# Kernel optimization log

Measured on AMD Instinct MI355X. Metric: run time of the kernel, lower is better.

## Reference

```python
import jax, jax.numpy as jnp
import numpy as np
from jax import lax

B, L, H, O, T = 256, 2, 256, 256, 512


def setup_inputs() -> dict:
    key = jax.random.key(0)
    ks = jax.random.split(key, 9)
    s = 0.1  # keep gates out of saturation
    return {
        "x": jax.random.normal(ks[0], (B, 1, H), jnp.float32),
        "h0": jax.random.normal(ks[1], (L, B, H), jnp.float32) * s,
        "c0": jax.random.normal(ks[2], (L, B, H), jnp.float32) * s,
        "W_ih": jax.random.normal(ks[3], (L, 4 * H, H), jnp.float32) * s,
        "W_hh": jax.random.normal(ks[4], (L, 4 * H, H), jnp.float32) * s,
        "b_ih": jax.random.normal(ks[5], (L, 4 * H), jnp.float32) * s,
        "b_hh": jax.random.normal(ks[6], (L, 4 * H), jnp.float32) * s,
        "fc_w": jax.random.normal(ks[7], (O, H), jnp.float32) * s,
        "fc_b": jax.random.normal(ks[8], (O,), jnp.float32) * s,
        "max_length": T,
    }


def _lstm_cell(inp, h, c, Wi, Wh, bi, bh):
    # PyTorch gate order: i, f, g, o
    gates = inp @ Wi.T + h @ Wh.T + bi + bh  # [B, 4H]
    i, f, g, o = jnp.split(gates, 4, axis=-1)
    i = jax.nn.sigmoid(i)
    f = jax.nn.sigmoid(f)
    g = jnp.tanh(g)
    o = jax.nn.sigmoid(o)
    c_new = f * c + i * g
    h_new = o * jnp.tanh(c_new)
    return h_new, c_new


def reference(x, h0, c0, W_ih, W_hh, b_ih, b_hh, fc_w, fc_b, max_length):
    n_layers = W_ih.shape[0]
    xin = x[:, 0, :]  # same single-step input re-fed every iteration

    def step(carry, _):
        h, c = carry  # each [L, B, H]
        inp = xin
        hs, cs = [], []
        for l in range(n_layers):
            hl, cl = _lstm_cell(inp, h[l], c[l], W_ih[l], W_hh[l], b_ih[l], b_hh[l])
            hs.append(hl)
            cs.append(cl)
            inp = hl
        return (jnp.stack(hs), jnp.stack(cs)), inp  # last-layer hidden

    _, outs = lax.scan(step, (h0, c0), None, length=max_length)  # [T, B, H]
    seq = jnp.transpose(outs, (1, 0, 2))  # [B, T, H]
    logits = seq @ fc_w.T + fc_b  # [B, T, O]
    return jax.nn.log_softmax(logits, axis=-1), jax.nn.softmax(logits, axis=-1)
```

## Files before the change

kernel.cpp:

```cpp
#include <hip/hip_runtime.h>

#define TSTEPS 512
#define BATCH  256
#define HID    256
#define OUTC   256

typedef _Float16 half8 __attribute__((ext_vector_type(8)));
typedef float    f32x4 __attribute__((ext_vector_type(4)));
union G16 { unsigned long long u2[2]; unsigned u[4]; half8 h; };

#define H0_SLOTS 16
#define H1_SLOTS 4
#define H0RING_QW (H0_SLOTS*16*16*128)
#define H1RING_QW (H1_SLOTS*16*16*128)

__device__ __forceinline__ float sigf(float x){ return 1.0f/(1.0f+__expf(-x)); }
__device__ __forceinline__ float tanh_(float x){
  float a = fminf(fmaxf(x,-8.0f),8.0f);
  float e = __expf(2.0f*a);
  return (e-1.0f)/(e+1.0f);
}
__device__ __forceinline__ void st64(unsigned long long* p, unsigned long long v){
  __hip_atomic_store(p, v, __ATOMIC_RELAXED, __HIP_MEMORY_SCOPE_AGENT);
}
__device__ __forceinline__ unsigned long long ld64(const unsigned long long* p){
  return __hip_atomic_load(p, __ATOMIC_RELAXED, __HIP_MEMORY_SCOPE_AGENT);
}
__device__ __forceinline__ void st32(unsigned* p, unsigned v){
  __hip_atomic_store(p, v, __ATOMIC_RELAXED, __HIP_MEMORY_SCOPE_AGENT);
}
__device__ __forceinline__ unsigned ld32(const unsigned* p){
  return __hip_atomic_load(p, __ATOMIC_RELAXED, __HIP_MEMORY_SCOPE_AGENT);
}
__device__ __forceinline__ unsigned pack2(float a, float b){
  _Float16 x=(_Float16)a, y=(_Float16)b;
  return (unsigned)__builtin_bit_cast(unsigned short,x)
       | ((unsigned)__builtin_bit_cast(unsigned short,y)<<16);
}

__global__ void prep_convert(const float* __restrict__ Wih, const float* __restrict__ Whh,
                             const float* __restrict__ fcw, const float* __restrict__ bih,
                             const float* __restrict__ bhh,
                             _Float16* __restrict__ wh0, _Float16* __restrict__ wi1,
                             _Float16* __restrict__ wh1, _Float16* __restrict__ fcwh,
                             float* __restrict__ bias1)
{
  int i = blockIdx.x*256 + threadIdx.x;
  wh0[i] = (_Float16)Whh[i];
  wi1[i] = (_Float16)Wih[262144 + i];
  wh1[i] = (_Float16)Whh[262144 + i];
  if (i < 65536) fcwh[i] = (_Float16)fcw[i];
  if (i < 1024)  bias1[i] = bih[1024+i] + bhh[1024+i];
}

__global__ void prep_gx0(const float* __restrict__ x, const float* __restrict__ Wih,
                         const float* __restrict__ bih, const float* __restrict__ bhh,
                         float* __restrict__ gx0)
{
  int gid = blockIdx.x*256 + threadIdx.x;
  int b = gid >> 10, n = gid & 1023;
  const float4* xv = (const float4*)(x + (size_t)b*256);
  const float4* wv = (const float4*)(Wih + (size_t)n*256);
  float s = bih[n] + bhh[n];
  #pragma unroll 8
  for (int k=0;k<64;k++){
    float4 a = xv[k], c = wv[k];
    s += a.x*c.x + a.y*c.y + a.z*c.z + a.w*c.w;
  }
  gx0[gid] = s;
}

__global__ void zero_scratch(unsigned long long* __restrict__ base, int total){
  int i = blockIdx.x*256 + threadIdx.x;
  if (i < total) st64(base + i, 0ull);
}

__global__ __launch_bounds__(512,1) void lstm4(
    const float* __restrict__ gx0, const _Float16* __restrict__ Wh0g,
    const _Float16* __restrict__ Wi1g, const _Float16* __restrict__ Wh1g,
    const float* __restrict__ bias1, const float* __restrict__ h_in,
    const float* __restrict__ c_in, unsigned* __restrict__ seq1dw,
    unsigned long long* __restrict__ h0r, unsigned long long* __restrict__ h1r,
    unsigned* __restrict__ flagC)
{
  __shared__ __align__(16) char Lb[156160];
  _Float16* Ws  = (_Float16*)Lb;
  _Float16* sh0 = (_Float16*)(Lb + 131072);

  const int blk = blockIdx.x, tid = threadIdx.x;
  const int wv = tid>>6, l = tid&63, c16 = l&15, kg = l>>4;

  if (blk < 64){
    const int grp = blk>>2, s = blk&3, b0 = grp*16;
    const int gate = wv>>1, jblk = (wv&1)*32;
    float (*gbuf)[16][66] = (float (*)[16][66])(Lb + 139264);

    for (int idx=tid; idx<8192; idx+=512){
      int row = idx>>5, gr = idx&31;
      int g = row>>6, jl = row&63;
      half8 v = *(const half8*)(Wh0g + ((size_t)(g*256 + s*64 + jl))*256 + gr*8);
      *(half8*)&Ws[row*256 + (gr^(row&7))*8] = v;
    }
    { int row = tid>>5, q = tid&31;
      const float* sp = h_in + (size_t)(b0+row)*256 + q*8;
      half8 v;
      #pragma unroll
      for (int qq=0;qq<8;qq++) v[qq] = (_Float16)sp[qq];
      *(half8*)&sh0[row*256 + (q^(row&7))*8] = v; }
    const int eb = tid>>5, jp = tid&31;
    float cA = c_in[(size_t)(b0+eb)*256 + s*64 + 2*jp];
    float cB = c_in[(size_t)(b0+eb)*256 + s*64 + 2*jp + 1];
    float gxr[2][4];
    #pragma unroll
    for (int nt=0;nt<2;nt++)
      #pragma unroll
      for (int r=0;r<4;r++)
        gxr[nt][r] = gx0[(size_t)(b0 + kg*4 + r)*1024 + gate*256 + s*64 + jblk + nt*16 + c16];
    const int r0 = gate*64 + jblk + c16, r1 = r0 + 16;
    __syncthreads();

    for (int t=0; t<TSTEPS; ++t){
      if (((t&7)==0) && t>=16 && tid<64){
        const unsigned need = (unsigned)(t-8);
        bool ok;
        do {
          unsigned v = need;
          if (tid < 8) v = ld32(&flagC[grp*8 + tid]);
          ok = (v >= need);
        } while (!__all(ok));
      }
      f32x4 acc0 = { gxr[0][0], gxr[0][1], gxr[0][2], gxr[0][3] };
      f32x4 acc1 = { gxr[1][0], gxr[1][1], gxr[1][2], gxr[1][3] };
      #pragma unroll
      for (int kt=0;kt<8;kt++){
        half8 af  = *(const half8*)&sh0[c16*256 + ((kt*4+kg)^(c16&7))*8];
        half8 b0f = *(const half8*)&Ws[r0*256 + ((kt*4+kg)^(r0&7))*8];
        half8 b1f = *(const half8*)&Ws[r1*256 + ((kt*4+kg)^(r1&7))*8];
        acc0 = __builtin_amdgcn_mfma_f32_16x16x32_f16(af, b0f, acc0, 0,0,0);
        acc1 = __builtin_amdgcn_mfma_f32_16x16x32_f16(af, b1f, acc1, 0,0,0);
      }
      #pragma unroll
      for (int r=0;r<4;r++){
        gbuf[gate][kg*4+r][jblk + c16]      = acc0[r];
        gbuf[gate][kg*4+r][jblk + 16 + c16] = acc1[r];
      }
      __syncthreads();
      {
        int j0 = 2*jp, j1 = 2*jp+1;
        float i0 = sigf (gbuf[0][eb][j0]), i1 = sigf (gbuf[0][eb][j1]);
        float f0 = sigf (gbuf[1][eb][j0]), f1 = sigf (gbuf[1][eb][j1]);
        float g0 = tanh_(gbuf[2][eb][j0]), g1 = tanh_(gbuf[2][eb][j1]);
        float o0 = sigf (gbuf[3][eb][j0]), o1 = sigf (gbuf[3][eb][j1]);
        cA = f0*cA + i0*g0;
        cB = f1*cB + i1*g1;
        unsigned pk = pack2(o0*tanh_(cA), o1*tanh_(cB));
        int jg = s*64 + j0;
        *(unsigned*)&sh0[eb*256 + ((jg>>3)^(eb&7))*8 + (jg&7)] = pk;
        st64(&h0r[(((size_t)(t&(H0_SLOTS-1))*16+grp)*16 + eb)*128 + s*32 + jp],
             (((unsigned long long)(unsigned)(t+2))<<32) | pk);
      }
      {
        int row = tid>>5, q = tid&31;
        if ((q>>3) != s){
          const unsigned long long* p =
            h0r + (((size_t)(t&(H0_SLOTS-1))*16+grp)*16 + row)*128 + q*4;
          unsigned tg32 = (unsigned)(t+2);
          unsigned long long v0,v1,v2,v3;
          for(;;){
            v0=ld64(p); v1=ld64(p+1); v2=ld64(p+2); v3=ld64(p+3);
            bool ok = (unsigned)(v0>>32)==tg32 && (unsigned)(v1>>32)==tg32 &&
                      (unsigned)(v2>>32)==tg32 && (unsigned)(v3>>32)==tg32;
            if (__all(ok)) break;
          }
          G16 g; g.u[0]=(unsigned)v0; g.u[1]=(unsigned)v1;
                 g.u[2]=(unsigned)v2; g.u[3]=(unsigned)v3;
          *(half8*)&sh0[row*256 + (q^(row&7))*8] = g.h;
        }
      }
      __syncthreads();
    }
  } else {
    const int bb = blk-64, grp = bb>>3, js = bb&7;
    const int b0 = grp*16, jb = js*32;
    const int gate = wv>>1, jhalf = (wv&1)*16;
    _Float16* sh1 = (_Float16*)(Lb + 139264);
    float (*gbuf)[16][34] = (float (*)[16][34])(Lb + 147456);

    for (int idx=tid; idx<8192; idx+=512){
      int row = idx>>6, gr = idx&63;
      int g = row>>5, jl = row&31;
      size_t nrow = (size_t)(g*256 + jb + jl);
      const _Float16* src = (gr < 32) ? (Wi1g + nrow*256 + gr*8)
                                      : (Wh1g + nrow*256 + (size_t)(gr-32)*8);
      *(half8*)&Ws[row*512 + (gr^(row&7))*8] = *(const half8*)src;
    }
    { int row = tid>>5, q = tid&31;
      const float* sp = h_in + 65536 + (size_t)(b0+row)*256 + q*8;
      half8 v;
      #pragma unroll
      for (int qq=0;qq<8;qq++) v[qq] = (_Float16)sp[qq];
      *(half8*)&sh1[row*256 + (q^(row&7))*8] = v; }
    const int eb = tid>>4, jp = tid&15;
    float cA = 0.f, cB = 0.f;
    if (tid < 256){
      cA = c_in[65536 + (size_t)(b0+eb)*256 + jb + 2*jp];
      cB = c_in[65536 + (size_t)(b0+eb)*256 + jb + 2*jp + 1];
    }
    const float bv = bias1[gate*256 + jb + jhalf + c16];
    const int nl = gate*32 + jhalf + c16;
    const int prow = tid>>5, pq = tid&31;
    unsigned long long hv0,hv1,hv2,hv3;
    {
      const unsigned long long* p = h0r + (((size_t)grp)*16 + prow)*128 + pq*4;
      hv0=ld64(p); hv1=ld64(p+1); hv2=ld64(p+2); hv3=ld64(p+3);
    }
    __syncthreads();

    for (int t=0; t<TSTEPS; ++t){
      {
        unsigned tg32 = (unsigned)(t+2);
        const unsigned long long* p =
          h0r + (((size_t)(t&(H0_SLOTS-1))*16+grp)*16 + prow)*128 + pq*4;
        for(;;){
          bool ok = (unsigned)(hv0>>32)==tg32 && (unsigned)(hv1>>32)==tg32 &&
                    (unsigned)(hv2>>32)==tg32 && (unsigned)(hv3>>32)==tg32;
          if (__all(ok)) break;
          hv0=ld64(p); hv1=ld64(p+1); hv2=ld64(p+2); hv3=ld64(p+3);
        }
        G16 g; g.u[0]=(unsigned)hv0; g.u[1]=(unsigned)hv1;
               g.u[2]=(unsigned)hv2; g.u[3]=(unsigned)hv3;
        *(half8*)&sh0[prow*256 + (pq^(prow&7))*8] = g.h;
      }
      __syncthreads();
      if (((t&7)==0) && tid==0) st32(&flagC[grp*8+js], (unsigned)t);
      f32x4 acc = { bv, bv, bv, bv };
      #pragma unroll
      for (int kt=0;kt<8;kt++){
        half8 af = *(const half8*)&sh0[c16*256 + ((kt*4+kg)^(c16&7))*8];
        half8 bf = *(const half8*)&Ws[nl*512 + ((kt*4+kg)^(nl&7))*8];
        acc = __builtin_amdgcn_mfma_f32_16x16x32_f16(af, bf, acc, 0,0,0);
      }
      if (t > 0 && (pq>>2) != js){
        const unsigned long long* p =
          h1r + (((size_t)((t+3)&(H1_SLOTS-1))*16+grp)*16 + prow)*128 + pq*4;
        unsigned tg32 = (unsigned)(t+1);
        unsigned long long v0,v1,v2,v3;
        for(;;){
          v0=ld64(p); v1=ld64(p+1); v2=ld64(p+2); v3=ld64(p+3);
          bool ok = (unsigned)(v0>>32)==tg32 && (unsigned)(v1>>32)==tg32 &&
                    (unsigned)(v2>>32)==tg32 && (unsigned)(v3>>32)==tg32;
          if (__all(ok)) break;
        }
        G16 g; g.u[0]=(unsigned)v0; g.u[1]=(unsigned)v1;
               g.u[2]=(unsigned)v2; g.u[3]=(unsigned)v3;
        *(half8*)&sh1[prow*256 + (pq^(prow&7))*8] = g.h;
      }
      __syncthreads();
      #pragma unroll
      for (int kt=0;kt<8;kt++){
        half8 af = *(const half8*)&sh1[c16*256 + ((kt*4+kg)^(c16&7))*8];
        half8 bf = *(const half8*)&Ws[nl*512 + ((32+kt*4+kg)^(nl&7))*8];
        acc = __builtin_amdgcn_mfma_f32_16x16x32_f16(af, bf, acc, 0,0,0);
      }
      #pragma unroll
      for (int r=0;r<4;r++) gbuf[gate][kg*4+r][jhalf + c16] = acc[r];
      __syncthreads();
      if (tid < 256){
        int j0 = 2*jp, j1 = 2*jp+1;
        float i0 = sigf (gbuf[0][eb][j0]), i1 = sigf (gbuf[0][eb][j1]);
        float f0 = sigf (gbuf[1][eb][j0]), f1 = sigf (gbuf[1][eb][j1]);
        float g0 = tanh_(gbuf[2][eb][j0]), g1 = tanh_(gbuf[2][eb][j1]);
        float o0 = sigf (gbuf[3][eb][j0]), o1 = sigf (gbuf[3][eb][j1]);
        cA = f0*cA + i0*g0;
        cB = f1*cB + i1*g1;
        unsigned pk = pack2(o0*tanh_(cA), o1*tanh_(cB));
        int jg = jb + j0;
        *(unsigned*)&sh1[eb*256 + ((jg>>3)^(eb&7))*8 + (jg&7)] = pk;
        st64(&h1r[(((size_t)(t&(H1_SLOTS-1))*16+grp)*16 + eb)*128 + js*16 + jp],
             (((unsigned long long)(unsigned)(t+2))<<32) | pk);
        seq1dw[((size_t)(b0+eb)*TSTEPS + t)*256 + js*16 + jp] = pk;
      }
      if (t+1 < TSTEPS){
        const unsigned long long* p =
          h0r + (((size_t)((t+1)&(H0_SLOTS-1))*16+grp)*16 + prow)*128 + pq*4;
        hv0=ld64(p); hv1=ld64(p+1); hv2=ld64(p+2); hv3=ld64(p+3);
      }
    }
  }
}

__global__ __launch_bounds__(256) void fc_kernel(
    const _Float16* __restrict__ seq, int pitch,
    const _Float16* __restrict__ fcwh, const float* __restrict__ fcb,
    float* __restrict__ out0, float* __restrict__ out1)
{
  const int tid = threadIdx.x;
  const int w = tid >> 6, l = tid & 63;
  const int col = l & 15, kg = l >> 4;
  const size_t m0 = (size_t)blockIdx.x*64 + (size_t)w*16;
  half8 a[8];
  #pragma unroll
  for (int kt=0;kt<8;kt++)
    a[kt] = *(const half8*)&seq[(m0+col)*(size_t)pitch + kt*32 + kg*8];
  f32x4 acc[16];
  #pragma unroll
  for (int nt=0;nt<16;nt++){
    int n = nt*16 + col;
    float bvl = fcb[n];
    f32x4 c = {bvl,bvl,bvl,bvl};
    const _Float16* wr = fcwh + (size_t)n*256;
    #pragma unroll
    for (int kt=0;kt<8;kt++){
      half8 bf = *(const half8*)&wr[kt*32 + kg*8];
      c = __builtin_amdgcn_mfma_f32_16x16x32_f16(a[kt], bf, c, 0,0,0);
    }
    acc[nt] = c;
  }
  #pragma unroll
  for (int r=0;r<4;r++){
    float mx = -3.0e38f;
    #pragma unroll
    for (int nt=0;nt<16;nt++) mx = fmaxf(mx, acc[nt][r]);
    #pragma unroll
    for (int off=1; off<16; off<<=1) mx = fmaxf(mx, __shfl_xor(mx, off, 64));
    float s = 0.0f;
    #pragma unroll
    for (int nt=0;nt<16;nt++) s += __expf(acc[nt][r]-mx);
    #pragma unroll
    for (int off=1; off<16; off<<=1) s += __shfl_xor(s, off, 64);
    float inv = 1.0f/s;
    float ls  = __logf(s);
    size_t row = m0 + (size_t)kg*4 + r;
    #pragma unroll
    for (int nt=0;nt<16;nt++){
      int n = nt*16 + col;
      float v = acc[nt][r]-mx;
      out0[row*256 + n] = v - ls;
      out1[row*256 + n] = __expf(v)*inv;
    }
  }
}

extern "C" void kernel_launch(void* const* d_in, const int* in_sizes, int n_in,
                              void* d_out, int out_size, void* d_ws, size_t ws_size,
                              hipStream_t stream)
{
  const float* x   = (const float*)d_in[0];
  const float* h0  = (const float*)d_in[1];
  const float* c0  = (const float*)d_in[2];
  const float* Wih = (const float*)d_in[3];
  const float* Whh = (const float*)d_in[4];
  const float* bih = (const float*)d_in[5];
  const float* bhh = (const float*)d_in[6];
  const float* fcw = (const float*)d_in[7];
  const float* fcb = (const float*)d_in[8];
  (void)in_sizes; (void)n_in; (void)out_size; (void)ws_size;

  char* ws = (char*)d_ws;
  _Float16* wh0   = (_Float16*)(ws + 0);
  _Float16* wi1   = (_Float16*)(ws + (512<<10));
  _Float16* wh1   = (_Float16*)(ws + (1024<<10));
  _Float16* fcwh  = (_Float16*)(ws + (1536<<10));
  float*    bias1 = (float*)   (ws + (1664<<10));
  float*    gx0   = (float*)   (ws + (1668<<10));

  char* ob = (char*)d_out;
  float* out0 = (float*)d_out;
  float* out1 = out0 + (size_t)BATCH*TSTEPS*OUTC;
  unsigned long long* h0r   = (unsigned long long*)ob;
  unsigned long long* h1r   = h0r + H0RING_QW;
  unsigned*           flagC = (unsigned*)(h1r + H1RING_QW);
  unsigned* seq1dw = (unsigned*)out1;
  _Float16* seq1   = (_Float16*)out1;

  const int zeroQW = H0RING_QW + H1RING_QW + 64;
  hipLaunchKernelGGL(zero_scratch, dim3((zeroQW+255)/256), dim3(256), 0, stream,
                     h0r, zeroQW);
  hipLaunchKernelGGL(prep_convert, dim3(1024), dim3(256), 0, stream,
                     Wih, Whh, fcw, bih, bhh, wh0, wi1, wh1, fcwh, bias1);
  hipLaunchKernelGGL(prep_gx0, dim3(1024), dim3(256), 0, stream,
                     x, Wih, bih, bhh, gx0);
  hipLaunchKernelGGL(lstm4, dim3(192), dim3(512), 0, stream,
                     gx0, wh0, wi1, wh1, bias1, h0, c0,
                     seq1dw, h0r, h1r, flagC);
  hipLaunchKernelGGL(fc_kernel, dim3(2048), dim3(256), 0, stream,
                     seq1, 512, fcwh, fcb, out0, out1);
}
```

Before: 1.810 ms.

## Replace tagged 64-bit hidden-state ring with plain fp16 ring plus per-slot flags

Blocks no longer exchange hidden state as 64-bit words carrying a step tag in the upper half. They write packed fp16 h values with sc1 stores, wait for the stores, barrier, and then publish a single per-slot flag. Consumers spin only on a few flag words and then read the ring with one 128-bit load per thread. This halves ring traffic and replaces wide polling of the data itself with flag polling. In exchange it adds extra block barriers per step, and all spin loops are capped at an iteration limit, so a slow producer could be skipped silently.

Result: slower. 1.905 ms (+5.3%).

```diff
diff --git a/kernel.cpp b/kernel.cpp
--- a/kernel.cpp
+++ b/kernel.cpp
@@ -7,12 +7,11 @@
 
 typedef _Float16 half8 __attribute__((ext_vector_type(8)));
 typedef float    f32x4 __attribute__((ext_vector_type(4)));
-union G16 { unsigned long long u2[2]; unsigned u[4]; half8 h; };
+typedef int      i32x4 __attribute__((ext_vector_type(4)));
 
 #define H0_SLOTS 16
 #define H1_SLOTS 4
-#define H0RING_QW (H0_SLOTS*16*16*128)
-#define H1RING_QW (H1_SLOTS*16*16*128)
+#define SPIN_CAP 65536
 
 __device__ __forceinline__ float sigf(float x){ return 1.0f/(1.0f+__expf(-x)); }
 __device__ __forceinline__ float tanh_(float x){
@@ -20,17 +19,20 @@
   float e = __expf(2.0f*a);
   return (e-1.0f)/(e+1.0f);
 }
-__device__ __forceinline__ void st64(unsigned long long* p, unsigned long long v){
+__device__ __forceinline__ void st32a(unsigned* p, unsigned v){
   __hip_atomic_store(p, v, __ATOMIC_RELAXED, __HIP_MEMORY_SCOPE_AGENT);
 }
-__device__ __forceinline__ unsigned long long ld64(const unsigned long long* p){
+__device__ __forceinline__ unsigned ld32a(const unsigned* p){
   return __hip_atomic_load(p, __ATOMIC_RELAXED, __HIP_MEMORY_SCOPE_AGENT);
 }
-__device__ __forceinline__ void st32(unsigned* p, unsigned v){
-  __hip_atomic_store(p, v, __ATOMIC_RELAXED, __HIP_MEMORY_SCOPE_AGENT);
-}
-__device__ __forceinline__ unsigned ld32(const unsigned* p){
-  return __hip_atomic_load(p, __ATOMIC_RELAXED, __HIP_MEMORY_SCOPE_AGENT);
+__device__ __forceinline__ void st32_sc1(void* p, unsigned v){
+  asm volatile("global_store_dword %0, %1, off sc1" :: "v"(p), "v"(v) : "memory");
+}
+__device__ __forceinline__ half8 ld128_sc1(const void* p){
+  i32x4 r;
+  asm volatile("global_load_dwordx4 %0, %1, off sc1\n\ts_waitcnt vmcnt(0)"
+               : "=&v"(r) : "v"(p) : "memory");
+  return __builtin_bit_cast(half8, r);
 }
 __device__ __forceinline__ unsigned pack2(float a, float b){
   _Float16 x=(_Float16)a, y=(_Float16)b;
@@ -70,17 +72,18 @@
   gx0[gid] = s;
 }
 
-__global__ void zero_scratch(unsigned long long* __restrict__ base, int total){
+__global__ void zero_flags(unsigned* __restrict__ f, int total){
   int i = blockIdx.x*256 + threadIdx.x;
-  if (i < total) st64(base + i, 0ull);
-}
-
-__global__ __launch_bounds__(512,1) void lstm4(
+  if (i < total) f[i] = 0u;
+}
+
+__global__ __launch_bounds__(512,1) void lstm7(
     const float* __restrict__ gx0, const _Float16* __restrict__ Wh0g,
     const _Float16* __restrict__ Wi1g, const _Float16* __restrict__ Wh1g,
     const float* __restrict__ bias1, const float* __restrict__ h_in,
     const float* __restrict__ c_in, unsigned* __restrict__ seq1dw,
-    unsigned long long* __restrict__ h0r, unsigned long long* __restrict__ h1r,
+    _Float16* __restrict__ h0r, _Float16* __restrict__ h1r,
+    unsigned* __restrict__ h0flag, unsigned* __restrict__ h1flag,
     unsigned* __restrict__ flagC)
 {
   __shared__ __align__(16) char Lb[156160];
@@ -120,14 +123,14 @@
     __syncthreads();
 
     for (int t=0; t<TSTEPS; ++t){
+      const int slot = t & (H0_SLOTS-1);
       if (((t&7)==0) && t>=16 && tid<64){
         const unsigned need = (unsigned)(t-8);
-        bool ok;
-        do {
+        for (int it=0; it<SPIN_CAP; ++it){
           unsigned v = need;
-          if (tid < 8) v = ld32(&flagC[grp*8 + tid]);
-          ok = (v >= need);
-        } while (!__all(ok));
+          if (tid < 8) v = ld32a(&flagC[grp*8 + tid]);
+          if (__all(v >= need)) break;
+        }
       }
       f32x4 acc0 = { gxr[0][0], gxr[0][1], gxr[0][2], gxr[0][3] };
       f32x4 acc1 = { gxr[1][0], gxr[1][1], gxr[1][2], gxr[1][3] };
@@ -154,30 +157,28 @@
         cA = f0*cA + i0*g0;
         cB = f1*cB + i1*g1;
         unsigned pk = pack2(o0*tanh_(cA), o1*tanh_(cB));
-        int jg = s*64 + j0;
-        *(unsigned*)&sh0[eb*256 + ((jg>>3)^(eb&7))*8 + (jg&7)] = pk;
-        st64(&h0r[(((size_t)(t&(H0_SLOTS-1))*16+grp)*16 + eb)*128 + s*32 + jp],
-             (((unsigned long long)(unsigned)(t+2))<<32) | pk);
-      }
-      {
-        int row = tid>>5, q = tid&31;
-        if ((q>>3) != s){
-          const unsigned long long* p =
-            h0r + (((size_t)(t&(H0_SLOTS-1))*16+grp)*16 + row)*128 + q*4;
-          unsigned tg32 = (unsigned)(t+2);
-          unsigned long long v0,v1,v2,v3;
-          for(;;){
-            v0=ld64(p); v1=ld64(p+1); v2=ld64(p+2); v3=ld64(p+3);
-            bool ok = (unsigned)(v0>>32)==tg32 && (unsigned)(v1>>32)==tg32 &&
-                      (unsigned)(v2>>32)==tg32 && (unsigned)(v3>>32)==tg32;
-            if (__all(ok)) break;
+        st32_sc1(&h0r[(((size_t)slot*16+grp)*16 + eb)*256 + s*64 + 2*jp], pk);
+      }
+      asm volatile("s_waitcnt vmcnt(0)" ::: "memory");
+      __syncthreads();
+      if (tid == 0) st32a(&h0flag[(grp*16+slot)*4 + s], (unsigned)(t+2));
+      if (t+1 < TSTEPS){
+        if (tid < 64){
+          const unsigned want = (unsigned)(t+2);
+          for (int it=0; it<SPIN_CAP; ++it){
+            unsigned v = want;
+            if (tid < 4 && tid != s) v = ld32a(&h0flag[(grp*16+slot)*4 + tid]);
+            if (__all(v == want)) break;
           }
-          G16 g; g.u[0]=(unsigned)v0; g.u[1]=(unsigned)v1;
-                 g.u[2]=(unsigned)v2; g.u[3]=(unsigned)v3;
-          *(half8*)&sh0[row*256 + (q^(row&7))*8] = g.h;
-        }
-      }
-      __syncthreads();
+        }
+        __syncthreads();
+        {
+          int row = tid>>5, q = tid&31;
+          half8 v = ld128_sc1(&h0r[(((size_t)slot*16+grp)*16 + row)*256 + q*8]);
+          *(half8*)&sh0[row*256 + (q^(row&7))*8] = v;
+        }
+        __syncthreads();
+      }
     }
   } else {
     const int bb = blk-64, grp = bb>>3, js = bb&7;
@@ -208,31 +209,25 @@
     }
     const float bv = bias1[gate*256 + jb + jhalf + c16];
     const int nl = gate*32 + jhalf + c16;
-    const int prow = tid>>5, pq = tid&31;
-    unsigned long long hv0,hv1,hv2,hv3;
-    {
-      const unsigned long long* p = h0r + (((size_t)grp)*16 + prow)*128 + pq*4;
-      hv0=ld64(p); hv1=ld64(p+1); hv2=ld64(p+2); hv3=ld64(p+3);
-    }
     __syncthreads();
 
     for (int t=0; t<TSTEPS; ++t){
-      {
-        unsigned tg32 = (unsigned)(t+2);
-        const unsigned long long* p =
-          h0r + (((size_t)(t&(H0_SLOTS-1))*16+grp)*16 + prow)*128 + pq*4;
-        for(;;){
-          bool ok = (unsigned)(hv0>>32)==tg32 && (unsigned)(hv1>>32)==tg32 &&
-                    (unsigned)(hv2>>32)==tg32 && (unsigned)(hv3>>32)==tg32;
-          if (__all(ok)) break;
-          hv0=ld64(p); hv1=ld64(p+1); hv2=ld64(p+2); hv3=ld64(p+3);
-        }
-        G16 g; g.u[0]=(unsigned)hv0; g.u[1]=(unsigned)hv1;
-               g.u[2]=(unsigned)hv2; g.u[3]=(unsigned)hv3;
-        *(half8*)&sh0[prow*256 + (pq^(prow&7))*8] = g.h;
-      }
-      __syncthreads();
-      if (((t&7)==0) && tid==0) st32(&flagC[grp*8+js], (unsigned)t);
+      const int slot  = t & (H0_SLOTS-1);
+      if (tid < 64){
+        const unsigned want = (unsigned)(t+2);
+        for (int it=0; it<SPIN_CAP; ++it){
+          unsigned v = want;
+          if (tid < 4) v = ld32a(&h0flag[(grp*16+slot)*4 + tid]);
+          if (__all(v == want)) break;
+        }
+      }
+      __syncthreads();
+      { int row = tid>>5, q = tid&31;
+        half8 v = ld128_sc1(&h0r[(((size_t)slot*16+grp)*16 + row)*256 + q*8]);
+        *(half8*)&sh0[row*256 + (q^(row&7))*8] = v;
+      }
+      __syncthreads();
+      if (((t&7)==0) && tid==0) st32a(&flagC[grp*8+js], (unsigned)t);
       f32x4 acc = { bv, bv, bv, bv };
       #pragma unroll
       for (int kt=0;kt<8;kt++){
@@ -240,20 +235,21 @@
         half8 bf = *(const half8*)&Ws[nl*512 + ((kt*4+kg)^(nl&7))*8];
         acc = __builtin_amdgcn_mfma_f32_16x16x32_f16(af, bf, acc, 0,0,0);
       }
-      if (t > 0 && (pq>>2) != js){
-        const unsigned long long* p =
-          h1r + (((size_t)((t+3)&(H1_SLOTS-1))*16+grp)*16 + prow)*128 + pq*4;
-        unsigned tg32 = (unsigned)(t+1);
-        unsigned long long v0,v1,v2,v3;
-        for(;;){
-          v0=ld64(p); v1=ld64(p+1); v2=ld64(p+2); v3=ld64(p+3);
-          bool ok = (unsigned)(v0>>32)==tg32 && (unsigned)(v1>>32)==tg32 &&
-                    (unsigned)(v2>>32)==tg32 && (unsigned)(v3>>32)==tg32;
-          if (__all(ok)) break;
-        }
-        G16 g; g.u[0]=(unsigned)v0; g.u[1]=(unsigned)v1;
-               g.u[2]=(unsigned)v2; g.u[3]=(unsigned)v3;
-        *(half8*)&sh1[prow*256 + (pq^(prow&7))*8] = g.h;
+      if (t > 0){
+        const int ps = (t-1) & (H1_SLOTS-1);
+        if (tid < 64){
+          const unsigned want = (unsigned)(t+1);
+          for (int it=0; it<SPIN_CAP; ++it){
+            unsigned v = want;
+            if (tid < 8 && tid != js) v = ld32a(&h1flag[(grp*4+ps)*8 + tid]);
+            if (__all(v == want)) break;
+          }
+        }
+        __syncthreads();
+        { int row = tid>>5, q = tid&31;
+          half8 v = ld128_sc1(&h1r[(((size_t)ps*16+grp)*16 + row)*256 + q*8]);
+          *(half8*)&sh1[row*256 + (q^(row&7))*8] = v;
+        }
       }
       __syncthreads();
       #pragma unroll
@@ -274,17 +270,13 @@
         cA = f0*cA + i0*g0;
         cB = f1*cB + i1*g1;
         unsigned pk = pack2(o0*tanh_(cA), o1*tanh_(cB));
-        int jg = jb + j0;
-        *(unsigned*)&sh1[eb*256 + ((jg>>3)^(eb&7))*8 + (jg&7)] = pk;
-        st64(&h1r[(((size_t)(t&(H1_SLOTS-1))*16+grp)*16 + eb)*128 + js*16 + jp],
-             (((unsigned long long)(unsigned)(t+2))<<32) | pk);
+        st32_sc1(&h1r[(((size_t)(t&(H1_SLOTS-1))*16+grp)*16 + eb)*256 + jb + 2*jp], pk);
         seq1dw[((size_t)(b0+eb)*TSTEPS + t)*256 + js*16 + jp] = pk;
       }
-      if (t+1 < TSTEPS){
-        const unsigned long long* p =
-          h0r + (((size_t)((t+1)&(H0_SLOTS-1))*16+grp)*16 + prow)*128 + pq*4;
-        hv0=ld64(p); hv1=ld64(p+1); hv2=ld64(p+2); hv3=ld64(p+3);
-      }
+      asm volatile("s_waitcnt vmcnt(0)" ::: "memory");
+      __syncthreads();
+      if (tid == 0)
+        st32a(&h1flag[(grp*4+(t&(H1_SLOTS-1)))*8 + js], (unsigned)(t+2));
     }
   }
 }
@@ -367,22 +359,22 @@
   char* ob = (char*)d_out;
   float* out0 = (float*)d_out;
   float* out1 = out0 + (size_t)BATCH*TSTEPS*OUTC;
-  unsigned long long* h0r   = (unsigned long long*)ob;
-  unsigned long long* h1r   = h0r + H0RING_QW;
-  unsigned*           flagC = (unsigned*)(h1r + H1RING_QW);
+  _Float16* h0r    = (_Float16*)ob;
+  _Float16* h1r    = (_Float16*)(ob + (2<<20));
+  unsigned* h0flag = (unsigned*)(ob + (3<<20));
+  unsigned* h1flag = h0flag + 1024;
+  unsigned* flagC  = h0flag + 1536;
   unsigned* seq1dw = (unsigned*)out1;
   _Float16* seq1   = (_Float16*)out1;
 
-  const int zeroQW = H0RING_QW + H1RING_QW + 64;
-  hipLaunchKernelGGL(zero_scratch, dim3((zeroQW+255)/256), dim3(256), 0, stream,
-                     h0r, zeroQW);
+  hipLaunchKernelGGL(zero_flags, dim3(7), dim3(256), 0, stream, h0flag, 1664);
   hipLaunchKernelGGL(prep_convert, dim3(1024), dim3(256), 0, stream,
                      Wih, Whh, fcw, bih, bhh, wh0, wi1, wh1, fcwh, bias1);
   hipLaunchKernelGGL(prep_gx0, dim3(1024), dim3(256), 0, stream,
                      x, Wih, bih, bhh, gx0);
-  hipLaunchKernelGGL(lstm4, dim3(192), dim3(512), 0, stream,
+  hipLaunchKernelGGL(lstm7, dim3(192), dim3(512), 0, stream,
                      gx0, wh0, wi1, wh1, bias1, h0, c0,
-                     seq1dw, h0r, h1r, flagC);
+                     seq1dw, h0r, h1r, h0flag, h1flag, flagC);
   hipLaunchKernelGGL(fc_kernel, dim3(2048), dim3(256), 0, stream,
                      seq1, 512, fcwh, fcb, out0, out1);
 }
```
